# Performance work log

Measured on AMD Instinct MI355X. Metric: run time of the kernel, lower is better.

Reference implementation:

```python
import jax, jax.numpy as jnp
import numpy as np

N = 8192
G = 12972
EPS = 1e-5


def setup_inputs() -> dict:
    key = jax.random.key(0)
    ks = jax.random.split(key, 8)
    # solutions: one-hot letters per position -> (N, 26, 5)
    sol_letters = jax.random.randint(ks[0], (N, 5), 0, 26)
    sols = jax.nn.one_hot(sol_letters, 26, dtype=jnp.float32).transpose(0, 2, 1)
    # guess vocabulary: one-hot words -> (G, 130) with (26,5) layout flattened
    g_letters = jax.random.randint(ks[1], (G, 5), 0, 26)
    guesses_mat = jax.nn.one_hot(g_letters, 26, dtype=jnp.float32).transpose(0, 2, 1).reshape(G, 130)
    s0 = 1.0 / np.sqrt(292.0)
    sh = 1.0 / np.sqrt(1000.0)
    W0 = jax.random.normal(ks[2], (292, 1000), jnp.float32) * s0
    b0 = jnp.zeros((1000,), jnp.float32)
    gammas = jnp.ones((4, 1000), jnp.float32)
    betas = jnp.zeros((4, 1000), jnp.float32)
    Wh = jax.random.normal(ks[3], (3, 1000, 1000), jnp.float32) * sh
    bh = jnp.zeros((3, 1000), jnp.float32)
    Wout = jax.random.normal(ks[4], (1000, 130), jnp.float32) * sh
    bout = jnp.zeros((130,), jnp.float32)
    return {"sols": sols, "guesses_mat": guesses_mat, "W0": W0, "b0": b0,
            "gammas": gammas, "betas": betas, "Wh": Wh, "bh": bh,
            "Wout": Wout, "bout": bout}


def _mlp(X, W0, b0, gammas, betas, Wh, bh, Wout, bout):
    h = X @ W0 + b0
    for i in range(4):
        mu = h.mean(axis=0)
        var = ((h - mu) ** 2).mean(axis=0)  # biased variance, as torch BN training
        h = gammas[i] * (h - mu) * jax.lax.rsqrt(var + EPS) + betas[i]
        h = jnp.where(h >= 0, h, 0.2 * h)
        if i < 3:
            h = h @ Wh[i] + bh[i]
        else:
            h = h @ Wout + bout
    return h


def reference(sols, guesses_mat, W0, b0, gammas, betas, Wh, bh, Wout, bout):
    n = sols.shape[0]
    hints = jnp.zeros((n, 286), jnp.float32)
    scores = 7.0 * jnp.ones((n,), jnp.float32)
    total_loss = jnp.float32(0.0)
    first_guess = None
    solved = jnp.zeros((n,), bool)
    sols_letters = jnp.clip(sols.sum(axis=2), 0.0, 1.0)[:, :, None]  # (n,26,1)
    for turn in range(6):
        turn_vec = jnp.zeros((n, 6), jnp.float32).at[:, turn].set(1.0)
        X = jnp.concatenate((hints, turn_vec), axis=1)  # (n, 292)
        y = _mlp(X, W0, b0, gammas, betas, Wh, bh, Wout, bout).reshape(n, 26, 5)
        logp = jax.nn.log_softmax(y, axis=1)
        loss = -(sols * logp).sum(axis=1).mean()
        if turn >= 1:
            total_loss = total_loss + loss
        y_soft = jax.nn.softmax(y, axis=1).reshape(n, 130)
        # nearest-guess retrieval: argmax over vocab of dot products, then gather
        sim = y_soft @ guesses_mat.T  # (n, G)
        idx = jnp.argmax(sim, axis=1)
        nudges = jax.lax.stop_gradient(guesses_mat[idx] - y_soft)
        guesses = (y_soft + nudges).reshape(n, 26, 5)
        if turn == 0:
            first_guess = guesses[0]
        greens = guesses * sols
        yellows = (1.0 - greens) * (guesses * sols_letters)
        blacks = (guesses * (1.0 - greens) * (1.0 - yellows)).sum(axis=2)  # (n,26)
        solved = greens.reshape(n, -1).sum(axis=1) == 5.0
        new_hints = jnp.concatenate((greens.reshape(n, 130), yellows.reshape(n, 130), blacks), axis=1)
        hints = hints + new_hints
        scores = jnp.where((scores > turn + 1) & solved, jnp.float32(turn + 1), scores)
    return total_loss, scores.sum(), solved.sum(), first_guess
```

## Files before the change

kernel.cpp:

```cpp
#include <hip/hip_runtime.h>

#define NROWS 8192
#define NG    12972
#define H     1000
#define NP    1024
#define KX    288
#define OCP   256
#define OC    130
#define EPSBN 1e-5f
#define MBLK  (NROWS / 128)

typedef __attribute__((ext_vector_type(8))) _Float16 f16x8;
typedef __attribute__((ext_vector_type(8))) unsigned short u16x8;
typedef __attribute__((ext_vector_type(4))) float f32x4;

__device__ __forceinline__ float lrelu(float x) { return x >= 0.f ? x : 0.2f * x; }

__global__ void transpose_f16(const float* __restrict__ src, int R, int C, int srcStride,
                              _Float16* __restrict__ dst, int Rp, int Cp) {
    __shared__ float tile[32][33];
    int k0 = blockIdx.x * 32;
    int n0 = blockIdx.y * 32;
    int tx = threadIdx.x, ty = threadIdx.y;
#pragma unroll
    for (int i = 0; i < 32; i += 8) {
        int k = k0 + ty + i, n = n0 + tx;
        tile[ty + i][tx] = (k < R && n < C) ? src[(size_t)k * srcStride + n] : 0.f;
    }
    __syncthreads();
#pragma unroll
    for (int i = 0; i < 32; i += 8) {
        int n = n0 + ty + i, k = k0 + tx;
        if (n < Cp && k < Rp) dst[(size_t)n * Rp + k] = (_Float16)tile[tx][ty + i];
    }
}

__global__ void prep_bias(const float* __restrict__ W0, const float* __restrict__ b0,
                          const float* __restrict__ bh, const float* __restrict__ bout,
                          float* __restrict__ b0p, float* __restrict__ w0t,
                          float* __restrict__ bhp, float* __restrict__ boutp) {
    int i = blockIdx.x * 256 + threadIdx.x;
    if (i < 1024) { b0p[i] = (i < H) ? b0[i] : 0.f; return; }
    i -= 1024;
    if (i < 6 * 1024) {
        int t = i >> 10, n = i & 1023;
        w0t[i] = (n < H) ? W0[(size_t)(286 + t) * H + n] : 0.f;
        return;
    }
    i -= 6 * 1024;
    if (i < 3 * 1024) {
        int l = i >> 10, n = i & 1023;
        bhp[i] = (n < H) ? bh[l * H + n] : 0.f;
        return;
    }
    i -= 3 * 1024;
    if (i < OCP) { boutp[i] = (i < OC) ? bout[i] : 0.f; }
}

__global__ void prep_guess_letters(const float* __restrict__ gm, unsigned char* __restrict__ gl,
                                   uint2* __restrict__ glp) {
    int g = blockIdx.x * blockDim.x + threadIdx.x;
    if (g >= NG) return;
    unsigned off[5];
    for (int p = 0; p < 5; ++p) {
        int letter = 0;
        for (int c = 0; c < 26; ++c)
            if (gm[(size_t)g * 130 + c * 5 + p] > 0.5f) { letter = c; break; }
        gl[g * 8 + p] = (unsigned char)letter;
        off[p] = (unsigned)(letter * 5 + p);
    }
    gl[g * 8 + 5] = gl[g * 8 + 6] = gl[g * 8 + 7] = 0;
    glp[g] = make_uint2(off[0] | (off[1] << 8) | (off[2] << 16) | (off[3] << 24), off[4]);
}

__global__ void prep_sol_letters(const float* __restrict__ sols, unsigned char* __restrict__ sl,
                                 unsigned int* __restrict__ msk) {
    int r = blockIdx.x * blockDim.x + threadIdx.x;
    if (r >= NROWS) return;
    unsigned int m = 0;
    for (int p = 0; p < 5; ++p) {
        int letter = 0;
        for (int c = 0; c < 26; ++c)
            if (sols[(size_t)r * 130 + c * 5 + p] > 0.5f) { letter = c; break; }
        sl[r * 8 + p] = (unsigned char)letter;
        m |= 1u << letter;
    }
    sl[r * 8 + 5] = sl[r * 8 + 6] = sl[r * 8 + 7] = 0;
    msk[r] = m;
}

__global__ void init_state(unsigned short* __restrict__ hX, float* __restrict__ scores,
                           int* __restrict__ solvedf, float* __restrict__ lossacc) {
    int i = blockIdx.x * blockDim.x + threadIdx.x;
    if (i < NROWS * KX) hX[i] = 0;
    if (i < NROWS) { scores[i] = 7.f; solvedf[i] = 0; }
    if (i == 0) lossacc[0] = 0.f;
}

template <int BK, bool HALF_C>
__global__ __launch_bounds__(256, 2) void gemm_f16(
    const _Float16* __restrict__ A, int lda,
    const _Float16* __restrict__ B, int ldb,
    void* __restrict__ Cv, int ldc,
    const float* __restrict__ bias1, const float* __restrict__ bias2, int kiter,
    float* __restrict__ pS, float* __restrict__ pS2) {
    constexpr int NCH = BK / 8;
    constexpr int ABYTES = 256 * BK;
    constexpr int KSUB = BK / 32;
    constexpr int AW = 16 * BK;
    __shared__ char smem[512 * BK];
    const int tid = threadIdx.x;
    const int lane = tid & 63;
    const int rowBase = blockIdx.x * 128;
    const int colBase = blockIdx.y * 128;
    const int wm = (tid >> 6) & 1;
    const int wn = tid >> 7;

    const _Float16* gsrc[NCH];
    int ldsuni[NCH];
#pragma unroll
    for (int i = 0; i < NCH; ++i) {
        int w = i * 256 + tid;
        const _Float16* plane;
        int off;
        if (w < AW) {
            int r = w & 127, kb = w >> 7;
            plane = A;
            off = (rowBase + r) * lda + kb * 8;
        } else {
            int v = w - AW;
            int col = v & 127, kb = v >> 7;
            plane = B;
            off = (colBase + col) * ldb + kb * 8;
        }
        gsrc[i] = plane + off;
        ldsuni[i] = (i * 256 + (tid & ~63)) * 16;
    }

    f32x4 acc[4][4];
    const f32x4 z = {0.f, 0.f, 0.f, 0.f};
#pragma unroll
    for (int m = 0; m < 4; ++m)
#pragma unroll
        for (int n = 0; n < 4; ++n) acc[m][n] = z;

    const int aro = (lane >> 4) * 2048 + (wm * 64 + (lane & 15)) * 16;
    const int bco = ABYTES + (lane >> 4) * 2048 + (wn * 64 + (lane & 15)) * 16;

    for (int t = 0; t < kiter; ++t) {
#pragma unroll
        for (int i = 0; i < NCH; ++i)
            __builtin_amdgcn_global_load_lds(
                (const __attribute__((address_space(1))) void*)(gsrc[i] + (size_t)t * BK),
                (__attribute__((address_space(3))) void*)(smem + ldsuni[i]), 16, 0, 0);
        __syncthreads();

        f16x8 a_f[KSUB][4], b_f[KSUB][4];
#pragma unroll
        for (int ks = 0; ks < KSUB; ++ks) {
#pragma unroll
            for (int m = 0; m < 4; ++m) a_f[ks][m] = *(const f16x8*)(smem + ks * 8192 + aro + m * 256);
#pragma unroll
            for (int n = 0; n < 4; ++n) b_f[ks][n] = *(const f16x8*)(smem + ks * 8192 + bco + n * 256);
        }
#pragma unroll
        for (int ks = 0; ks < KSUB; ++ks)
#pragma unroll
            for (int m = 0; m < 4; ++m)
#pragma unroll
                for (int n = 0; n < 4; ++n)
                    acc[m][n] = __builtin_amdgcn_mfma_f32_16x16x32_f16(a_f[ks][m], b_f[ks][n],
                                                                       acc[m][n], 0, 0, 0);
        __syncthreads();
    }

    float* sS  = (float*)smem;
    float* sS2 = (float*)smem + 256;
    const int lane16 = lane & 15, lanehi = lane >> 4;
#pragma unroll
    for (int n = 0; n < 4; ++n) {
        int col = colBase + wn * 64 + n * 16 + lane16;
        float bv = bias1[col] + (bias2 ? bias2[col] : 0.f);
        float s = 0.f, s2 = 0.f;
#pragma unroll
        for (int m = 0; m < 4; ++m) {
            int row0 = rowBase + wm * 64 + m * 16 + lanehi * 4;
#pragma unroll
            for (int r = 0; r < 4; ++r) {
                float cv = acc[m][n][r] + bv;
                if constexpr (HALF_C)
                    ((_Float16*)Cv)[(size_t)(row0 + r) * ldc + col] = (_Float16)cv;
                else
                    ((float*)Cv)[(size_t)(row0 + r) * ldc + col] = cv;
                s += cv; s2 += cv * cv;
            }
        }
        if (pS) {
            s += __shfl_xor(s, 16);  s += __shfl_xor(s, 32);
            s2 += __shfl_xor(s2, 16); s2 += __shfl_xor(s2, 32);
            if (lanehi == 0) {
                int lcol = wn * 64 + n * 16 + lane16;
                sS[wm * 128 + lcol] = s;
                sS2[wm * 128 + lcol] = s2;
            }
        }
    }
    if (pS) {
        __syncthreads();
        if (tid < 128) {
            int col = colBase + tid;
            pS[(size_t)blockIdx.x * NP + col] = sS[tid] + sS[128 + tid];
            pS2[(size_t)blockIdx.x * NP + col] = sS2[tid] + sS2[128 + tid];
        }
    }
}

__global__ __launch_bounds__(256) void bn_apply_f(
    const _Float16* __restrict__ hraw, const float* __restrict__ pS, const float* __restrict__ pS2,
    const float* __restrict__ gamma, const float* __restrict__ beta,
    _Float16* __restrict__ oh, int psjStride) {
    __shared__ float la[128], lb[128];
    const int tid = threadIdx.x;
    const int rowBase = blockIdx.x * 128;
    const int colBase = blockIdx.y * 128;
    if (tid < 128) {
        int col = colBase + tid;
        float s = 0.f;
        for (int j = 0; j < MBLK; ++j) s += pS[(size_t)j * psjStride + col];
        la[tid] = s;
    } else {
        int col = colBase + tid - 128;
        float s2 = 0.f;
        for (int j = 0; j < MBLK; ++j) s2 += pS2[(size_t)j * psjStride + col];
        lb[tid - 128] = s2;
    }
    __syncthreads();
    if (tid < 128) {
        int col = colBase + tid;
        float a = 0.f, b = 0.f;
        if (col < H) {
            float mean = la[tid] * (1.f / NROWS);
            float var = lb[tid] * (1.f / NROWS) - mean * mean;
            float inv = rsqrtf(var + EPSBN);
            a = gamma[col] * inv;
            b = beta[col] - mean * a;
        }
        la[tid] = a;
        lb[tid] = b;
    }
    __syncthreads();
    const int c8 = (tid & 15) * 8;
    float ar[8], br[8];
#pragma unroll
    for (int j = 0; j < 8; ++j) { ar[j] = la[c8 + j]; br[j] = lb[c8 + j]; }
#pragma unroll
    for (int i = 0; i < 8; ++i) {
        int row = i * 16 + (tid >> 4);
        const u16x8 v = *(const u16x8*)(hraw + (size_t)(rowBase + row) * NP + colBase + c8);
        u16x8 o;
#pragma unroll
        for (int j = 0; j < 8; ++j) {
            float x = (float)__builtin_bit_cast(_Float16, (unsigned short)v[j]);
            o[j] = __builtin_bit_cast(unsigned short, (_Float16)lrelu(ar[j] * x + br[j]));
        }
        *(u16x8*)((unsigned short*)oh + (size_t)(rowBase + row) * NP + colBase + c8) = o;
    }
}

__global__ __launch_bounds__(256) void post_turn(
    const float* __restrict__ ybuf, const uint2* __restrict__ glp,
    const unsigned char* __restrict__ gl, const unsigned char* __restrict__ sl,
    const unsigned int* __restrict__ msk, _Float16* __restrict__ hX,
    float* __restrict__ scores, int* __restrict__ solvedf, float* __restrict__ lossacc,
    const float* __restrict__ gm, float* __restrict__ dout, int turn) {
    const int r0 = blockIdx.x * 8;
    __shared__ float pk[8][132];
    __shared__ float lcon[40];
    __shared__ float wb[4][8];
    __shared__ int wi[4][8];
    __shared__ int fidx[8];
    const int tid = threadIdx.x;

    if (tid < 40) {
        int row = tid / 5, p = tid - row * 5;
        const float* yr = ybuf + (size_t)(r0 + row) * OCP + p;
        float m = -1e30f;
#pragma unroll
        for (int c = 0; c < 26; ++c) m = fmaxf(m, yr[c * 5]);
        float e[26];
        float s = 0.f;
#pragma unroll
        for (int c = 0; c < 26; ++c) { e[c] = expf(yr[c * 5] - m); s += e[c]; }
        float inv = 1.f / s;
#pragma unroll
        for (int c = 0; c < 26; ++c) pk[row][c * 5 + p] = e[c] * inv;
        lcon[tid] = logf(s) + m - yr[sl[(size_t)(r0 + row) * 8 + p] * 5];
    }
    __syncthreads();

    float bb[8];
    int ii[8];
#pragma unroll
    for (int r = 0; r < 8; ++r) { bb[r] = -1e30f; ii[r] = 1 << 30; }
    for (int g = tid; g < NG; g += 256) {
        uint2 w = glp[g];
        int o0 = w.x & 255, o1 = (w.x >> 8) & 255, o2 = (w.x >> 16) & 255,
            o3 = w.x >> 24, o4 = w.y & 255;
#pragma unroll
        for (int r = 0; r < 8; ++r) {
            float v = pk[r][o0] + pk[r][o1]; v += pk[r][o2]; v += pk[r][o3]; v += pk[r][o4];
            if (v > bb[r]) { bb[r] = v; ii[r] = g; }
        }
    }
#pragma unroll
    for (int off = 1; off < 64; off <<= 1) {
#pragma unroll
        for (int r = 0; r < 8; ++r) {
            float o = __shfl_xor(bb[r], off);
            int oi = __shfl_xor(ii[r], off);
            if (o > bb[r] || (o == bb[r] && oi < ii[r])) { bb[r] = o; ii[r] = oi; }
        }
    }
    const int wid = tid >> 6, lane = tid & 63;
    if (lane == 0) {
#pragma unroll
        for (int r = 0; r < 8; ++r) { wb[wid][r] = bb[r]; wi[wid][r] = ii[r]; }
    }
    __syncthreads();

    if (tid < 8) {
        float b = wb[0][tid]; int x = wi[0][tid];
#pragma unroll
        for (int wv = 1; wv < 4; ++wv)
            if (wb[wv][tid] > b || (wb[wv][tid] == b && wi[wv][tid] < x)) { b = wb[wv][tid]; x = wi[wv][tid]; }
        fidx[tid] = x;
        int r = r0 + tid;
        const unsigned char* q = gl + x * 8;
        const unsigned char* so = sl + (size_t)r * 8;
        unsigned int mk = msk[r];
        _Float16* hrow = hX + (size_t)r * KX;
        int allg = 1;
#pragma unroll
        for (int p = 0; p < 5; ++p) {
            int g = q[p];
            int off;
            if (g == so[p]) {
                off = g * 5 + p;
            } else {
                allg = 0;
                off = ((mk >> g) & 1u) ? (130 + g * 5 + p) : (260 + g);
            }
            hrow[off] = (_Float16)((float)hrow[off] + 1.f);
        }
        solvedf[r] = allg;
        if (allg && scores[r] > (float)(turn + 1)) scores[r] = (float)(turn + 1);
    }
    if (tid == 16 && turn >= 1) {
        float t = 0.f;
#pragma unroll
        for (int j = 0; j < 40; ++j) t += lcon[j];
        atomicAdd(lossacc, t * (1.f / (NROWS * 5)));
    }
    __syncthreads();
    if (turn == 0 && blockIdx.x == 0 && tid >= 64 && tid < 64 + OC) {
        dout[3 + tid - 64] = gm[(size_t)fidx[0] * OC + (tid - 64)];
    }
}

__global__ __launch_bounds__(256) void post_turn0(
    const float* __restrict__ ybuf, const uint2* __restrict__ glp,
    const float* __restrict__ gm, float* __restrict__ dout, int* __restrict__ idx0buf) {
    __shared__ float pk[132];
    __shared__ float wb[4];
    __shared__ int wi[4];
    __shared__ int fidx;
    const int tid = threadIdx.x;
    if (tid < 5) {
        int p = tid;
        const float* yr = ybuf + p;
        float m = -1e30f;
#pragma unroll
        for (int c = 0; c < 26; ++c) m = fmaxf(m, yr[c * 5]);
        float e[26];
        float s = 0.f;
#pragma unroll
        for (int c = 0; c < 26; ++c) { e[c] = expf(yr[c * 5] - m); s += e[c]; }
        float inv = 1.f / s;
#pragma unroll
        for (int c = 0; c < 26; ++c) pk[c * 5 + p] = e[c] * inv;
    }
    __syncthreads();
    float b = -1e30f;
    int bi = 1 << 30;
    for (int g = tid; g < NG; g += 256) {
        uint2 w = glp[g];
        int o0 = w.x & 255, o1 = (w.x >> 8) & 255, o2 = (w.x >> 16) & 255,
            o3 = w.x >> 24, o4 = w.y & 255;
        float v = pk[o0] + pk[o1]; v += pk[o2]; v += pk[o3]; v += pk[o4];
        if (v > b) { b = v; bi = g; }
    }
#pragma unroll
    for (int off = 1; off < 64; off <<= 1) {
        float o = __shfl_xor(b, off);
        int oi = __shfl_xor(bi, off);
        if (o > b || (o == b && oi < bi)) { b = o; bi = oi; }
    }
    const int wid = tid >> 6, lane = tid & 63;
    if (lane == 0) { wb[wid] = b; wi[wid] = bi; }
    __syncthreads();
    if (tid == 0) {
        float bx = wb[0]; int x = wi[0];
#pragma unroll
        for (int wv = 1; wv < 4; ++wv)
            if (wb[wv] > bx || (wb[wv] == bx && wi[wv] < x)) { bx = wb[wv]; x = wi[wv]; }
        fidx = x;
        idx0buf[0] = x;
    }
    __syncthreads();
    if (tid >= 64 && tid < 64 + OC) {
        dout[3 + tid - 64] = gm[(size_t)fidx * OC + (tid - 64)];
    }
}

__global__ void hints0(const int* __restrict__ idx0buf, const unsigned char* __restrict__ gl,
                       const unsigned char* __restrict__ sl, const unsigned int* __restrict__ msk,
                       _Float16* __restrict__ hX, float* __restrict__ scores,
                       int* __restrict__ solvedf) {
    int r = blockIdx.x * 256 + threadIdx.x;
    if (r >= NROWS) return;
    int x = idx0buf[0];
    const unsigned char* q = gl + x * 8;
    const unsigned char* so = sl + (size_t)r * 8;
    unsigned int mk = msk[r];
    _Float16* hrow = hX + (size_t)r * KX;
    int allg = 1;
#pragma unroll
    for (int p = 0; p < 5; ++p) {
        int g = q[p];
        int off;
        if (g == so[p]) {
            off = g * 5 + p;
        } else {
            allg = 0;
            off = ((mk >> g) & 1u) ? (130 + g * 5 + p) : (260 + g);
        }
        hrow[off] = (_Float16)((float)hrow[off] + 1.f);
    }
    solvedf[r] = allg;
    if (allg && scores[r] > 1.f) scores[r] = 1.f;
}

__global__ void final_reduce(const float* __restrict__ scores, const int* __restrict__ solvedf,
                             const float* __restrict__ lossacc, float* __restrict__ dout) {
    __shared__ float rs[256];
    __shared__ int ri[256];
    int tid = threadIdx.x;
    float s = 0.f;
    int c = 0;
    for (int r = tid; r < NROWS; r += 256) { s += scores[r]; c += solvedf[r]; }
    rs[tid] = s; ri[tid] = c;
    __syncthreads();
    for (int off = 128; off > 0; off >>= 1) {
        if (tid < off) { rs[tid] += rs[tid + off]; ri[tid] += ri[tid + off]; }
        __syncthreads();
    }
    if (tid == 0) {
        dout[0] = lossacc[0];
        dout[1] = rs[0];
        dout[2] = (float)ri[0];
    }
}

extern "C" void kernel_launch(void* const* d_in, const int* in_sizes, int n_in,
                              void* d_out, int out_size, void* d_ws, size_t ws_size,
                              hipStream_t stream) {
    const float* sols   = (const float*)d_in[0];
    const float* gm     = (const float*)d_in[1];
    const float* W0     = (const float*)d_in[2];
    const float* b0     = (const float*)d_in[3];
    const float* gammas = (const float*)d_in[4];
    const float* betas  = (const float*)d_in[5];
    const float* Wh     = (const float*)d_in[6];
    const float* bh     = (const float*)d_in[7];
    const float* Wout   = (const float*)d_in[8];
    const float* bout   = (const float*)d_in[9];
    float* dout = (float*)d_out;

    char* p = (char*)d_ws;
    auto alloc = [&](size_t bytes) { void* r = (void*)p; p += (bytes + 255) & ~(size_t)255; return r; };
    _Float16* hX   = (_Float16*)alloc((size_t)NROWS * KX * 2);
    _Float16* hA   = (_Float16*)alloc((size_t)NROWS * NP * 2);
    _Float16* hraw = (_Float16*)alloc((size_t)NROWS * NP * 2);
    float* ybuf    = (float*)alloc((size_t)NROWS * OCP * 4);
    _Float16* B0T = (_Float16*)alloc((size_t)NP * KX * 2);
    _Float16* WhT = (_Float16*)alloc((size_t)3 * NP * NP * 2);
    _Float16* BoT = (_Float16*)alloc((size_t)OCP * NP * 2);
    float* b0p   = (float*)alloc(NP * 4);
    float* w0t   = (float*)alloc(6 * NP * 4);
    float* bhp   = (float*)alloc(3 * NP * 4);
    float* boutp = (float*)alloc(OCP * 4);
    float* pS    = (float*)alloc((size_t)MBLK * NP * 4);
    float* pS2   = (float*)alloc((size_t)MBLK * NP * 4);
    float* scores  = (float*)alloc(NROWS * 4);
    float* lossacc = (float*)alloc(256);
    int* solvedf = (int*)alloc(NROWS * 4);
    int* idx0buf = (int*)alloc(256);
    unsigned char* gl = (unsigned char*)alloc(NG * 8);
    uint2* glp = (uint2*)alloc(NG * 8);
    unsigned char* sl = (unsigned char*)alloc(NROWS * 8);
    unsigned int* msk = (unsigned int*)alloc(NROWS * 4);

    transpose_f16<<<dim3(KX / 32, NP / 32), dim3(32, 8), 0, stream>>>(W0, 286, H, H, B0T, KX, NP);
    for (int l = 0; l < 3; ++l)
        transpose_f16<<<dim3(NP / 32, NP / 32), dim3(32, 8), 0, stream>>>(
            Wh + (size_t)l * H * H, H, H, H, WhT + (size_t)l * NP * NP, NP, NP);
    transpose_f16<<<dim3(NP / 32, OCP / 32), dim3(32, 8), 0, stream>>>(Wout, H, OC, OC, BoT, NP, OCP);
    prep_bias<<<41, 256, 0, stream>>>(W0, b0, bh, bout, b0p, w0t, bhp, boutp);
    prep_guess_letters<<<(NG + 255) / 256, 256, 0, stream>>>(gm, gl, glp);
    prep_sol_letters<<<(NROWS + 255) / 256, 256, 0, stream>>>(sols, sl, msk);
    init_state<<<(NROWS * KX + 255) / 256, 256, 0, stream>>>((unsigned short*)hX, scores, solvedf, lossacc);

    for (int t = 0; t < 6; ++t) {
        const int mg = (t == 0) ? 1 : MBLK;
        const int psStride = (t == 0) ? 0 : NP;
        gemm_f16<32, true><<<dim3(mg, NP / 128), 256, 0, stream>>>(
            hX, KX, B0T, KX, hraw, NP, b0p, w0t + t * NP, KX / 32, pS, pS2);
        for (int l = 0; l < 4; ++l) {
            bn_apply_f<<<dim3(mg, NP / 128), 256, 0, stream>>>(
                hraw, pS, pS2, gammas + (size_t)l * H, betas + (size_t)l * H, hA, psStride);
            if (l < 3) {
                gemm_f16<64, true><<<dim3(mg, NP / 128), 256, 0, stream>>>(
                    hA, NP, WhT + (size_t)l * NP * NP, NP, hraw, NP, bhp + l * NP, nullptr,
                    NP / 64, pS, pS2);
            } else {
                gemm_f16<64, false><<<dim3(mg, OCP / 128), 256, 0, stream>>>(
                    hA, NP, BoT, NP, ybuf, OCP, boutp, nullptr, NP / 64, nullptr, nullptr);
            }
        }
        if (t == 0) {
            post_turn0<<<1, 256, 0, stream>>>(ybuf, glp, gm, dout, idx0buf);
            hints0<<<NROWS / 256, 256, 0, stream>>>(idx0buf, gl, sl, msk, hX, scores, solvedf);
        } else {
            post_turn<<<NROWS / 8, 256, 0, stream>>>(ybuf, glp, gl, sl, msk, hX, scores, solvedf,
                                                     lossacc, gm, dout, t);
        }
    }
    final_reduce<<<1, 256, 0, stream>>>(scores, solvedf, lossacc, dout);
}
```

Baseline: 1.487 ms.

## Add 64-row output GEMM and pack softmax pairs in argmax scan

The final 1000->130 output projection now uses a dedicated kernel with 64-row tiles. This doubles the block count for the small-N GEMM so more of the GPU is occupied, at the cost of reloading the B tile more often. Separately, the guess-retrieval scan in post_turn stores the softmax probabilities of row pairs as float2. Each vocabulary letter lookup then fetches two rows with one LDS read, halving the shared-memory load count in the argmax loop.

```diff
diff --git a/kernel.cpp b/kernel.cpp
--- a/kernel.cpp
+++ b/kernel.cpp
@@ -215,6 +215,92 @@
     }
 }
 
+__global__ __launch_bounds__(256, 2) void gemm_out64(
+    const _Float16* __restrict__ A, int lda,
+    const _Float16* __restrict__ B, int ldb,
+    float* __restrict__ C, int ldc,
+    const float* __restrict__ bias1, int kiter) {
+    constexpr int BK = 64;
+    __shared__ char smem[24576];
+    const int tid = threadIdx.x;
+    const int lane = tid & 63;
+    const int rowBase = blockIdx.x * 64;
+    const int colBase = blockIdx.y * 128;
+    const int wn = tid >> 6;
+
+    const _Float16* gsrc[6];
+    int ldsuni[6];
+#pragma unroll
+    for (int i = 0; i < 6; ++i) {
+        int w = i * 256 + tid;
+        const _Float16* plane;
+        int off;
+        if (w < 512) {
+            int r = w & 63, kb = w >> 6;
+            plane = A;
+            off = (rowBase + r) * lda + kb * 8;
+        } else {
+            int v = w - 512;
+            int col = v & 127, kb = v >> 7;
+            plane = B;
+            off = (colBase + col) * ldb + kb * 8;
+        }
+        gsrc[i] = plane + off;
+        ldsuni[i] = (i * 256 + (tid & ~63)) * 16;
+    }
+
+    f32x4 acc[4][2];
+    const f32x4 z = {0.f, 0.f, 0.f, 0.f};
+#pragma unroll
+    for (int m = 0; m < 4; ++m)
+#pragma unroll
+        for (int n = 0; n < 2; ++n) acc[m][n] = z;
+
+    const int aro = (lane >> 4) * 1024 + (lane & 15) * 16;
+    const int bco = 8192 + (lane >> 4) * 2048 + (wn * 32 + (lane & 15)) * 16;
+
+    for (int t = 0; t < kiter; ++t) {
+#pragma unroll
+        for (int i = 0; i < 6; ++i)
+            __builtin_amdgcn_global_load_lds(
+                (const __attribute__((address_space(1))) void*)(gsrc[i] + (size_t)t * BK),
+                (__attribute__((address_space(3))) void*)(smem + ldsuni[i]), 16, 0, 0);
+        __syncthreads();
+
+        f16x8 a_f[2][4], b_f[2][2];
+#pragma unroll
+        for (int ks = 0; ks < 2; ++ks) {
+#pragma unroll
+            for (int m = 0; m < 4; ++m) a_f[ks][m] = *(const f16x8*)(smem + ks * 4096 + aro + m * 256);
+#pragma unroll
+            for (int n = 0; n < 2; ++n) b_f[ks][n] = *(const f16x8*)(smem + ks * 8192 + bco + n * 256);
+        }
+#pragma unroll
+        for (int ks = 0; ks < 2; ++ks)
+#pragma unroll
+            for (int m = 0; m < 4; ++m)
+#pragma unroll
+                for (int n = 0; n < 2; ++n)
+                    acc[m][n] = __builtin_amdgcn_mfma_f32_16x16x32_f16(a_f[ks][m], b_f[ks][n],
+                                                                       acc[m][n], 0, 0, 0);
+        __syncthreads();
+    }
+
+    const int lane16 = lane & 15, lanehi = lane >> 4;
+#pragma unroll
+    for (int n = 0; n < 2; ++n) {
+        int col = colBase + wn * 32 + n * 16 + lane16;
+        float bv = bias1[col];
+#pragma unroll
+        for (int m = 0; m < 4; ++m) {
+            int row0 = rowBase + m * 16 + lanehi * 4;
+#pragma unroll
+            for (int r = 0; r < 4; ++r)
+                C[(size_t)(row0 + r) * ldc + col] = acc[m][n][r] + bv;
+        }
+    }
+}
+
 __global__ __launch_bounds__(256) void bn_apply_f(
     const _Float16* __restrict__ hraw, const float* __restrict__ pS, const float* __restrict__ pS2,
     const float* __restrict__ gamma, const float* __restrict__ beta,
@@ -274,7 +360,7 @@
     float* __restrict__ scores, int* __restrict__ solvedf, float* __restrict__ lossacc,
     const float* __restrict__ gm, float* __restrict__ dout, int turn) {
     const int r0 = blockIdx.x * 8;
-    __shared__ float pk[8][132];
+    __shared__ float2 pk2[4][132];
     __shared__ float lcon[40];
     __shared__ float wb[4][8];
     __shared__ int wi[4][8];
@@ -293,7 +379,8 @@
         for (int c = 0; c < 26; ++c) { e[c] = expf(yr[c * 5] - m); s += e[c]; }
         float inv = 1.f / s;
 #pragma unroll
-        for (int c = 0; c < 26; ++c) pk[row][c * 5 + p] = e[c] * inv;
+        for (int c = 0; c < 26; ++c)
+            ((float*)&pk2[row >> 1][c * 5 + p])[row & 1] = e[c] * inv;
         lcon[tid] = logf(s) + m - yr[sl[(size_t)(r0 + row) * 8 + p] * 5];
     }
     __syncthreads();
@@ -307,9 +394,16 @@
         int o0 = w.x & 255, o1 = (w.x >> 8) & 255, o2 = (w.x >> 16) & 255,
             o3 = w.x >> 24, o4 = w.y & 255;
 #pragma unroll
-        for (int r = 0; r < 8; ++r) {
-            float v = pk[r][o0] + pk[r][o1]; v += pk[r][o2]; v += pk[r][o3]; v += pk[r][o4];
-            if (v > bb[r]) { bb[r] = v; ii[r] = g; }
+        for (int tp = 0; tp < 4; ++tp) {
+            float2 s0 = pk2[tp][o0];
+            float2 s1 = pk2[tp][o1];
+            float2 s2 = pk2[tp][o2];
+            float2 s3 = pk2[tp][o3];
+            float2 s4 = pk2[tp][o4];
+            float vx = s0.x + s1.x; vx += s2.x; vx += s3.x; vx += s4.x;
+            float vy = s0.y + s1.y; vy += s2.y; vy += s3.y; vy += s4.y;
+            if (vx > bb[2 * tp]) { bb[2 * tp] = vx; ii[2 * tp] = g; }
+            if (vy > bb[2 * tp + 1]) { bb[2 * tp + 1] = vy; ii[2 * tp + 1] = g; }
         }
     }
 #pragma unroll
@@ -533,8 +627,8 @@
                     hA, NP, WhT + (size_t)l * NP * NP, NP, hraw, NP, bhp + l * NP, nullptr,
                     NP / 64, pS, pS2);
             } else {
-                gemm_f16<64, false><<<dim3(mg, OCP / 128), 256, 0, stream>>>(
-                    hA, NP, BoT, NP, ybuf, OCP, boutp, nullptr, NP / 64, nullptr, nullptr);
+                gemm_out64<<<dim3((t == 0) ? 1 : MBLK * 2, OCP / 128), 256, 0, stream>>>(
+                    hA, NP, BoT, NP, ybuf, OCP, boutp, NP / 64);
             }
         }
         if (t == 0) {
```

Result: slower. 1.539 ms (+3.5%).
